# Optimization experiments

Measured on AMD Instinct MI355X. Metric: run time of the kernel, lower is better.

The kernel has to match this reference:

```python
import jax, jax.numpy as jnp
import numpy as np


def setup_inputs() -> dict:
    key = jax.random.key(0)
    k1, k2, k3, k4, k5 = jax.random.split(key, 5)
    in_f, out_f, rank = 4096, 4096, 16
    std = 1.0 / np.sqrt(rank)
    x = jax.random.normal(k1, (4, 2048, in_f), dtype=jnp.float32)
    base_weight = jax.random.normal(k2, (out_f, in_f), dtype=jnp.float32) * 0.02
    lora_A = jax.random.normal(k3, (rank, in_f), dtype=jnp.float32) * std
    lora_B = jax.random.normal(k4, (out_f, rank), dtype=jnp.float32) * 0.01
    magnitude_vec = jax.random.uniform(k5, (out_f,), dtype=jnp.float32) + 0.5
    return {"x": x, "base_weight": base_weight, "lora_A": lora_A,
            "lora_B": lora_B, "magnitude_vec": magnitude_vec}


def reference(x, base_weight, lora_A, lora_B, magnitude_vec):
    # x: [B, S, in] -> tokens [N, in]
    out_shape = (*x.shape[:-1], base_weight.shape[0])
    xt = x.reshape(-1, x.shape[-1])
    # low-rank adapter path: [N, rank] @ [rank, out]
    lora_out = (xt @ lora_A.T) @ lora_B.T
    # column-wise L2 norm of adapted weight, per output row: [out]
    adapted_w = base_weight + lora_B @ lora_A
    column_norm = jnp.linalg.norm(adapted_w, axis=1)
    magnitude_scale = magnitude_vec / column_norm  # [out]
    # base GEMM + adapter + magnitude rescale epilogue
    dora_out = (xt @ base_weight.T + lora_out) * magnitude_scale[None, :]
    return dora_out.reshape(out_shape)
```

## Files before the change

kernel.cpp:

```cpp
#include <hip/hip_runtime.h>
#include <hip/hip_bf16.h>
#include <stdint.h>

typedef __attribute__((ext_vector_type(8))) short s16x8;
typedef __attribute__((ext_vector_type(4))) float f32x4;
typedef __attribute__((ext_vector_type(8))) unsigned short us8;
typedef __attribute__((ext_vector_type(4))) unsigned short us4;

__device__ inline unsigned short bf_rne(float f) {
    union { float f; uint32_t u; } v; v.f = f;
    uint32_t u = v.u;
    u += 0x7FFFu + ((u >> 16) & 1u);
    return (unsigned short)(u >> 16);
}

#define GLD_LDS16(gp, lp)                                                     \
    __builtin_amdgcn_global_load_lds(                                         \
        (const __attribute__((address_space(1))) void*)(gp),                  \
        (__attribute__((address_space(3))) void*)(lp), 16, 0, 0)

__global__ __launch_bounds__(256) void prologue_kernel(
    const float4* __restrict__ x4, us4* __restrict__ xbf4,
    const float4* __restrict__ W4,
    const float4* __restrict__ A4,
    const float* __restrict__ B,
    const float* __restrict__ mag,
    unsigned short* __restrict__ wbf,
    float* __restrict__ scale) {
    const int tid = threadIdx.x;
    if (blockIdx.x < 512) {
        const int m0 = blockIdx.x * 8;
        __shared__ float Bs[8][16];
        __shared__ float red[32];
        if (tid < 128) Bs[tid >> 4][tid & 15] = B[m0 * 16 + tid];
        __syncthreads();
        float ss[8] = {};
        for (int c = tid; c < 1024; c += 256) {
            float4 a[16];
#pragma unroll
            for (int r = 0; r < 16; ++r) a[r] = A4[r * 1024 + c];
#pragma unroll
            for (int i = 0; i < 8; ++i) {
                float4 w = W4[(size_t)(m0 + i) * 1024 + c];
#pragma unroll
                for (int r = 0; r < 16; ++r) {
                    const float br = Bs[i][r];
                    w.x += br * a[r].x; w.y += br * a[r].y;
                    w.z += br * a[r].z; w.w += br * a[r].w;
                }
                ss[i] += w.x * w.x + w.y * w.y + w.z * w.z + w.w * w.w;
                us4 o; o[0] = bf_rne(w.x); o[1] = bf_rne(w.y);
                o[2] = bf_rne(w.z); o[3] = bf_rne(w.w);
                *(us4*)&wbf[(size_t)(m0 + i) * 4096 + c * 4] = o;
            }
        }
        const int lane = tid & 63, wv = tid >> 6;
#pragma unroll
        for (int i = 0; i < 8; ++i) {
            float v = ss[i];
#pragma unroll
            for (int off = 32; off > 0; off >>= 1) v += __shfl_down(v, off, 64);
            if (lane == 0) red[wv * 8 + i] = v;
        }
        __syncthreads();
        if (tid < 8) {
            float tot = red[tid] + red[8 + tid] + red[16 + tid] + red[24 + tid];
            scale[m0 + tid] = mag[m0 + tid] / sqrtf(tot);
        }
    } else {
        const size_t base = (size_t)(blockIdx.x - 512) * 1024 + tid;
#pragma unroll
        for (int j = 0; j < 4; ++j) {
            const size_t idx = base + j * 256;
            float4 a = x4[idx];
            us4 o;
            o[0] = bf_rne(a.x); o[1] = bf_rne(a.y);
            o[2] = bf_rne(a.z); o[3] = bf_rne(a.w);
            xbf4[idx] = o;
        }
    }
}

#define FENCE() asm volatile("" ::: "memory")
#define BAR()   do { FENCE(); __builtin_amdgcn_s_barrier(); FENCE(); } while (0)
#define VMW6()  asm volatile("s_waitcnt vmcnt(6)" ::: "memory")
#define VMW0()  asm volatile("s_waitcnt vmcnt(0)" ::: "memory")
#define LGW8()  asm volatile("s_waitcnt lgkmcnt(8)" ::: "memory")
#define LGW0()  asm volatile("s_waitcnt lgkmcnt(0)" ::: "memory")
#define PRIO1() __builtin_amdgcn_s_setprio(1)
#define PRIO0() __builtin_amdgcn_s_setprio(0)

__global__ __launch_bounds__(512, 2) void dora_gemm(
    const unsigned short* __restrict__ xbf,
    const unsigned short* __restrict__ wbf,
    const float* __restrict__ scale,
    float* __restrict__ out) {
    __shared__ __align__(16) unsigned short As[2][256 * 64];
    __shared__ __align__(16) unsigned short Bs[2][256 * 64];

    const int tid  = threadIdx.x;
    const int lane = tid & 63;
    const int w    = tid >> 6;
    const int wm   = w >> 2;
    const int wn   = w & 3;
    const int q    = lane >> 4;
    const int c15  = lane & 15;

    const int bid = blockIdx.x;
    const int xcd = bid & 7, sub = bid >> 3;
    const int tileM = (((xcd & 3) << 3) | (sub & 7)) << 8;
    const int tileN = (((xcd >> 2) << 3) | (sub >> 3)) << 8;

    const int r0 = tid >> 3;
    const int lc = (tid & 7) ^ (r0 & 7);
    const size_t aoff = (size_t)(tileM + r0) * 4096 + lc * 8;
    const size_t boff = (size_t)(tileN + r0) * 4096 + lc * 8;
    const int ld0 = (w * 64) * 8;
    const int ld1 = (512 + w * 64) * 8;

#define STAGE_A(d, h, k0) do {                                                            \
    GLD_LDS16(xbf + aoff + (size_t)((h) * 128) * 4096 + (k0),      &As[d][(h) * 8192 + ld0]); \
    GLD_LDS16(xbf + aoff + (size_t)((h) * 128 + 64) * 4096 + (k0), &As[d][(h) * 8192 + ld1]); \
} while (0)
#define STAGE_B(d, h, k0) do {                                                            \
    GLD_LDS16(wbf + boff + (size_t)((h) * 128) * 4096 + (k0),      &Bs[d][(h) * 8192 + ld0]); \
    GLD_LDS16(wbf + boff + (size_t)((h) * 128 + 64) * 4096 + (k0), &Bs[d][(h) * 8192 + ld1]); \
} while (0)

    s16x8 af[4][2];
    s16x8 bfx[2][2][2];
    f32x4 acc[8][4] = {};

#define READ_A(d, mh) do {                                                    \
    _Pragma("unroll") for (int mt = 0; mt < 4; ++mt) {                        \
        const int row = (mh) * 128 + wm * 64 + mt * 16 + c15;                 \
        _Pragma("unroll") for (int kc = 0; kc < 2; ++kc) {                    \
            const int phys = (kc * 4 + q) ^ (row & 7);                        \
            af[mt][kc] = *(const s16x8*)&As[d][row * 64 + phys * 8];          \
        } } } while (0)
#define READ_B(d, nh) do {                                                    \
    _Pragma("unroll") for (int nt = 0; nt < 2; ++nt) {                        \
        const int row = (nh) * 128 + wn * 32 + nt * 16 + c15;                 \
        _Pragma("unroll") for (int kc = 0; kc < 2; ++kc) {                    \
            const int phys = (kc * 4 + q) ^ (row & 7);                        \
            bfx[nh][nt][kc] = *(const s16x8*)&Bs[d][row * 64 + phys * 8];     \
        } } } while (0)
#define MFMA_Q(mh, nh) do {                                                   \
    _Pragma("unroll") for (int mt = 0; mt < 4; ++mt)                          \
    _Pragma("unroll") for (int nt = 0; nt < 2; ++nt)                          \
    _Pragma("unroll") for (int kc = 0; kc < 2; ++kc)                          \
        acc[(mh) * 4 + mt][(nh) * 2 + nt] =                                   \
            __builtin_amdgcn_mfma_f32_16x16x32_bf16(                          \
                af[mt][kc], bfx[nh][nt][kc],                                  \
                acc[(mh) * 4 + mt][(nh) * 2 + nt], 0, 0, 0);                  \
} while (0)

    STAGE_A(0, 0, 0); STAGE_B(0, 0, 0); STAGE_B(0, 1, 0); STAGE_A(0, 1, 0);
    STAGE_A(1, 0, 64); STAGE_B(1, 0, 64); STAGE_B(1, 1, 64);
    VMW6(); BAR();

    for (int t0k = 0; t0k < 62 * 64; t0k += 128) {
        const int kA1 = t0k + 64;
        const int kn2 = t0k + 128;
        const int kn3 = t0k + 192;
        READ_A(0, 0); READ_B(0, 0);
        STAGE_A(1, 1, kA1);
        LGW8(); BAR(); LGW0();
        PRIO1(); MFMA_Q(0, 0); PRIO0(); BAR();
        READ_B(0, 1);
        STAGE_A(0, 0, kn2);
        BAR(); LGW0();
        PRIO1(); MFMA_Q(0, 1); PRIO0(); BAR();
        READ_A(0, 1);
        STAGE_B(0, 0, kn2);
        BAR(); LGW0();
        PRIO1(); MFMA_Q(1, 1); PRIO0(); BAR();
        STAGE_B(0, 1, kn2);
        VMW6(); BAR();
        PRIO1(); MFMA_Q(1, 0); PRIO0(); BAR();
        READ_A(1, 0); READ_B(1, 0);
        STAGE_A(0, 1, kn2);
        LGW8(); BAR(); LGW0();
        PRIO1(); MFMA_Q(0, 0); PRIO0(); BAR();
        READ_B(1, 1);
        STAGE_A(1, 0, kn3);
        BAR(); LGW0();
        PRIO1(); MFMA_Q(0, 1); PRIO0(); BAR();
        READ_A(1, 1);
        STAGE_B(1, 0, kn3);
        BAR(); LGW0();
        PRIO1(); MFMA_Q(1, 1); PRIO0(); BAR();
        STAGE_B(1, 1, kn3);
        VMW6(); BAR();
        PRIO1(); MFMA_Q(1, 0); PRIO0(); BAR();
    }

    READ_A(0, 0); READ_B(0, 0);
    STAGE_A(1, 1, 63 * 64);
    LGW8(); BAR(); LGW0();
    PRIO1(); MFMA_Q(0, 0); PRIO0(); BAR();
    READ_B(0, 1); BAR(); LGW0();
    PRIO1(); MFMA_Q(0, 1); PRIO0(); BAR();
    READ_A(0, 1); BAR(); LGW0();
    PRIO1(); MFMA_Q(1, 1); PRIO0(); BAR();
    VMW0(); BAR();
    PRIO1(); MFMA_Q(1, 0); PRIO0(); BAR();
    READ_A(1, 0); READ_B(1, 0); BAR(); LGW0();
    PRIO1(); MFMA_Q(0, 0); PRIO0(); BAR();
    READ_B(1, 1); BAR(); LGW0();
    PRIO1(); MFMA_Q(0, 1); PRIO0(); BAR();
    READ_A(1, 1); BAR(); LGW0();
    PRIO1(); MFMA_Q(1, 1); PRIO0();
    MFMA_Q(1, 0);

#pragma unroll
    for (int nh = 0; nh < 2; ++nh)
#pragma unroll
    for (int nt = 0; nt < 2; ++nt) {
        const int col = tileN + nh * 128 + wn * 32 + nt * 16 + c15;
        const float s = scale[col];
#pragma unroll
        for (int mh = 0; mh < 2; ++mh)
#pragma unroll
        for (int mt = 0; mt < 4; ++mt) {
            const int row0 = tileM + mh * 128 + wm * 64 + mt * 16 + q * 4;
#pragma unroll
            for (int r = 0; r < 4; ++r)
                out[(size_t)(row0 + r) * 4096 + col] = acc[mh * 4 + mt][nh * 2 + nt][r] * s;
        }
    }
}

extern "C" void kernel_launch(void* const* d_in, const int* in_sizes, int n_in,
                              void* d_out, int out_size, void* d_ws, size_t ws_size,
                              hipStream_t stream) {
    const float* x   = (const float*)d_in[0];
    const float* W   = (const float*)d_in[1];
    const float* A   = (const float*)d_in[2];
    const float* B   = (const float*)d_in[3];
    const float* mag = (const float*)d_in[4];
    float* out = (float*)d_out;

    const size_t XBF_BYTES = (size_t)8192 * 4096 * 2;
    const size_t WBF_BYTES = (size_t)4096 * 4096 * 2;
    const size_t NEEDED = XBF_BYTES + WBF_BYTES + 4096 * sizeof(float);
    if (ws_size < NEEDED) return;

    unsigned short* xbf = (unsigned short*)d_ws;
    unsigned short* wbf = (unsigned short*)((char*)d_ws + XBF_BYTES);
    float* scale = (float*)((char*)d_ws + XBF_BYTES + WBF_BYTES);

    prologue_kernel<<<8704, 256, 0, stream>>>((const float4*)x, (us4*)xbf,
                                              (const float4*)W, (const float4*)A,
                                              B, mag, wbf, scale);
    dora_gemm<<<512, 512, 0, stream>>>(xbf, wbf, scale, out);
}
```

Baseline: 357.4 us.

## Switch GEMM to 32x32x16 bf16 MFMA tiles with deferred LDS waits

Replaces the 16x16x32 MFMA tiling with 32x32x16 instructions. Each wave now computes 2x2 32x32 sub-tiles per quadrant with 16-wide accumulators, and the LDS fragment reads and epilogue row mapping are changed to match. The LDS wait and barrier are moved to after each MFMA group, so fragment reads for the next quadrant can overlap with matrix math. The aim is fewer MFMA issues and fewer LDS reads per flop. The cost is a different register layout, and correctness now depends on the reordered waits.

Result: slower. 369.1 us (+3.3%).

```diff
diff --git a/kernel.cpp b/kernel.cpp
--- a/kernel.cpp
+++ b/kernel.cpp
@@ -3,8 +3,7 @@
 #include <stdint.h>
 
 typedef __attribute__((ext_vector_type(8))) short s16x8;
-typedef __attribute__((ext_vector_type(4))) float f32x4;
-typedef __attribute__((ext_vector_type(8))) unsigned short us8;
+typedef __attribute__((ext_vector_type(16))) float f32x16;
 typedef __attribute__((ext_vector_type(4))) unsigned short us4;
 
 __device__ inline unsigned short bf_rne(float f) {
@@ -85,7 +84,6 @@
 #define BAR()   do { FENCE(); __builtin_amdgcn_s_barrier(); FENCE(); } while (0)
 #define VMW6()  asm volatile("s_waitcnt vmcnt(6)" ::: "memory")
 #define VMW0()  asm volatile("s_waitcnt vmcnt(0)" ::: "memory")
-#define LGW8()  asm volatile("s_waitcnt lgkmcnt(8)" ::: "memory")
 #define LGW0()  asm volatile("s_waitcnt lgkmcnt(0)" ::: "memory")
 #define PRIO1() __builtin_amdgcn_s_setprio(1)
 #define PRIO0() __builtin_amdgcn_s_setprio(0)
@@ -103,8 +101,8 @@
     const int w    = tid >> 6;
     const int wm   = w >> 2;
     const int wn   = w & 3;
-    const int q    = lane >> 4;
-    const int c15  = lane & 15;
+    const int r31  = lane & 31;
+    const int hi   = lane >> 5;
 
     const int bid = blockIdx.x;
     const int xcd = bid & 7, sub = bid >> 3;
@@ -127,32 +125,28 @@
     GLD_LDS16(wbf + boff + (size_t)((h) * 128 + 64) * 4096 + (k0), &Bs[d][(h) * 8192 + ld1]); \
 } while (0)
 
-    s16x8 af[4][2];
-    s16x8 bfx[2][2][2];
-    f32x4 acc[8][4] = {};
-
-#define READ_A(d, mh) do {                                                    \
-    _Pragma("unroll") for (int mt = 0; mt < 4; ++mt) {                        \
-        const int row = (mh) * 128 + wm * 64 + mt * 16 + c15;                 \
-        _Pragma("unroll") for (int kc = 0; kc < 2; ++kc) {                    \
-            const int phys = (kc * 4 + q) ^ (row & 7);                        \
+    s16x8 af[2][4];
+    s16x8 bfx[2][4];
+    f32x16 acc[4][2] = {};
+
+#define READ_A32(d, mh) do {                                                  \
+    _Pragma("unroll") for (int mt = 0; mt < 2; ++mt) {                        \
+        const int row = (mh) * 128 + wm * 64 + mt * 32 + r31;                 \
+        _Pragma("unroll") for (int kc = 0; kc < 4; ++kc) {                    \
+            const int phys = (kc * 2 + hi) ^ (row & 7);                       \
             af[mt][kc] = *(const s16x8*)&As[d][row * 64 + phys * 8];          \
         } } } while (0)
-#define READ_B(d, nh) do {                                                    \
-    _Pragma("unroll") for (int nt = 0; nt < 2; ++nt) {                        \
-        const int row = (nh) * 128 + wn * 32 + nt * 16 + c15;                 \
-        _Pragma("unroll") for (int kc = 0; kc < 2; ++kc) {                    \
-            const int phys = (kc * 4 + q) ^ (row & 7);                        \
-            bfx[nh][nt][kc] = *(const s16x8*)&Bs[d][row * 64 + phys * 8];     \
+#define READ_B32(d, nh) do {                                                  \
+    {   const int row = (nh) * 128 + wn * 32 + r31;                           \
+        _Pragma("unroll") for (int kc = 0; kc < 4; ++kc) {                    \
+            const int phys = (kc * 2 + hi) ^ (row & 7);                       \
+            bfx[nh][kc] = *(const s16x8*)&Bs[d][row * 64 + phys * 8];         \
         } } } while (0)
-#define MFMA_Q(mh, nh) do {                                                   \
-    _Pragma("unroll") for (int mt = 0; mt < 4; ++mt)                          \
-    _Pragma("unroll") for (int nt = 0; nt < 2; ++nt)                          \
-    _Pragma("unroll") for (int kc = 0; kc < 2; ++kc)                          \
-        acc[(mh) * 4 + mt][(nh) * 2 + nt] =                                   \
-            __builtin_amdgcn_mfma_f32_16x16x32_bf16(                          \
-                af[mt][kc], bfx[nh][nt][kc],                                  \
-                acc[(mh) * 4 + mt][(nh) * 2 + nt], 0, 0, 0);                  \
+#define MFMA_Q32(mh, nh) do {                                                 \
+    _Pragma("unroll") for (int kc = 0; kc < 4; ++kc)                          \
+    _Pragma("unroll") for (int mt = 0; mt < 2; ++mt)                          \
+        acc[(mh) * 2 + mt][nh] = __builtin_amdgcn_mfma_f32_32x32x16_bf16(     \
+            af[mt][kc], bfx[nh][kc], acc[(mh) * 2 + mt][nh], 0, 0, 0);        \
 } while (0)
 
     STAGE_A(0, 0, 0); STAGE_B(0, 0, 0); STAGE_B(0, 1, 0); STAGE_A(0, 1, 0);
@@ -163,70 +157,89 @@
         const int kA1 = t0k + 64;
         const int kn2 = t0k + 128;
         const int kn3 = t0k + 192;
-        READ_A(0, 0); READ_B(0, 0);
+        READ_A32(0, 0); READ_B32(0, 0);
         STAGE_A(1, 1, kA1);
-        LGW8(); BAR(); LGW0();
-        PRIO1(); MFMA_Q(0, 0); PRIO0(); BAR();
-        READ_B(0, 1);
+        BAR();
+        PRIO1(); MFMA_Q32(0, 0); PRIO0();
+        LGW0(); BAR();
+        READ_B32(0, 1);
         STAGE_A(0, 0, kn2);
-        BAR(); LGW0();
-        PRIO1(); MFMA_Q(0, 1); PRIO0(); BAR();
-        READ_A(0, 1);
+        BAR();
+        PRIO1(); MFMA_Q32(0, 1); PRIO0();
+        LGW0(); BAR();
+        READ_A32(0, 1);
         STAGE_B(0, 0, kn2);
-        BAR(); LGW0();
-        PRIO1(); MFMA_Q(1, 1); PRIO0(); BAR();
+        BAR();
+        PRIO1(); MFMA_Q32(1, 1); PRIO0();
+        LGW0(); BAR();
         STAGE_B(0, 1, kn2);
         VMW6(); BAR();
-        PRIO1(); MFMA_Q(1, 0); PRIO0(); BAR();
-        READ_A(1, 0); READ_B(1, 0);
+        PRIO1(); MFMA_Q32(1, 0); PRIO0();
+        BAR();
+        READ_A32(1, 0); READ_B32(1, 0);
         STAGE_A(0, 1, kn2);
-        LGW8(); BAR(); LGW0();
-        PRIO1(); MFMA_Q(0, 0); PRIO0(); BAR();
-        READ_B(1, 1);
+        BAR();
+        PRIO1(); MFMA_Q32(0, 0); PRIO0();
+        LGW0(); BAR();
+        READ_B32(1, 1);
         STAGE_A(1, 0, kn3);
-        BAR(); LGW0();
-        PRIO1(); MFMA_Q(0, 1); PRIO0(); BAR();
-        READ_A(1, 1);
+        BAR();
+        PRIO1(); MFMA_Q32(0, 1); PRIO0();
+        LGW0(); BAR();
+        READ_A32(1, 1);
         STAGE_B(1, 0, kn3);
-        BAR(); LGW0();
-        PRIO1(); MFMA_Q(1, 1); PRIO0(); BAR();
+        BAR();
+        PRIO1(); MFMA_Q32(1, 1); PRIO0();
+        LGW0(); BAR();
         STAGE_B(1, 1, kn3);
         VMW6(); BAR();
-        PRIO1(); MFMA_Q(1, 0); PRIO0(); BAR();
+        PRIO1(); MFMA_Q32(1, 0); PRIO0();
+        BAR();
     }
 
-    READ_A(0, 0); READ_B(0, 0);
+    READ_A32(0, 0); READ_B32(0, 0);
     STAGE_A(1, 1, 63 * 64);
-    LGW8(); BAR(); LGW0();
-    PRIO1(); MFMA_Q(0, 0); PRIO0(); BAR();
-    READ_B(0, 1); BAR(); LGW0();
-    PRIO1(); MFMA_Q(0, 1); PRIO0(); BAR();
-    READ_A(0, 1); BAR(); LGW0();
-    PRIO1(); MFMA_Q(1, 1); PRIO0(); BAR();
+    BAR();
+    PRIO1(); MFMA_Q32(0, 0); PRIO0();
+    LGW0(); BAR();
+    READ_B32(0, 1);
+    BAR();
+    PRIO1(); MFMA_Q32(0, 1); PRIO0();
+    LGW0(); BAR();
+    READ_A32(0, 1);
+    BAR();
+    PRIO1(); MFMA_Q32(1, 1); PRIO0();
+    LGW0(); BAR();
     VMW0(); BAR();
-    PRIO1(); MFMA_Q(1, 0); PRIO0(); BAR();
-    READ_A(1, 0); READ_B(1, 0); BAR(); LGW0();
-    PRIO1(); MFMA_Q(0, 0); PRIO0(); BAR();
-    READ_B(1, 1); BAR(); LGW0();
-    PRIO1(); MFMA_Q(0, 1); PRIO0(); BAR();
-    READ_A(1, 1); BAR(); LGW0();
-    PRIO1(); MFMA_Q(1, 1); PRIO0();
-    MFMA_Q(1, 0);
-
-#pragma unroll
-    for (int nh = 0; nh < 2; ++nh)
-#pragma unroll
-    for (int nt = 0; nt < 2; ++nt) {
-        const int col = tileN + nh * 128 + wn * 32 + nt * 16 + c15;
+    PRIO1(); MFMA_Q32(1, 0); PRIO0();
+    BAR();
+    READ_A32(1, 0); READ_B32(1, 0);
+    BAR();
+    PRIO1(); MFMA_Q32(0, 0); PRIO0();
+    LGW0(); BAR();
+    READ_B32(1, 1);
+    BAR();
+    PRIO1(); MFMA_Q32(0, 1); PRIO0();
+    LGW0(); BAR();
+    READ_A32(1, 1);
+    MFMA_Q32(1, 1);
+    MFMA_Q32(1, 0);
+
+#pragma unroll
+    for (int nh = 0; nh < 2; ++nh) {
+        const int col = tileN + nh * 128 + wn * 32 + r31;
         const float s = scale[col];
 #pragma unroll
         for (int mh = 0; mh < 2; ++mh)
 #pragma unroll
-        for (int mt = 0; mt < 4; ++mt) {
-            const int row0 = tileM + mh * 128 + wm * 64 + mt * 16 + q * 4;
-#pragma unroll
-            for (int r = 0; r < 4; ++r)
-                out[(size_t)(row0 + r) * 4096 + col] = acc[mh * 4 + mt][nh * 2 + nt][r] * s;
+        for (int mt = 0; mt < 2; ++mt) {
+            const int rbase = tileM + mh * 128 + wm * 64 + mt * 32 + hi * 4;
+            const f32x16 a = acc[mh * 2 + mt][nh];
+#pragma unroll
+            for (int reg = 0; reg < 16; ++reg) {
+                const int row = rbase + (reg & 3) + ((reg >> 2) << 3);
+                out[(size_t)row * 4096 + col] = a[reg] * s;
+            }
         }
     }
 }
```
